# Kernel optimization log

Hardware: AMD Instinct MI355X
Metric: run time of the kernel (lower is better)

## Reference

```python
import jax, jax.numpy as jnp
import numpy as np

PART = 0  # index of '<PART>' tag in vocab (select_part_tag = zeros)
W = 3     # max_word_len


def lstm_scan(x_seq, h0, c0, Wih, Whh, bih, bhh):
    """x_seq: [S, N, D] -> outputs [S, N, H]. torch LSTM gate order i, f, g, o."""
    def cell(carry, x):
        h, c = carry
        g = x @ Wih.T + bih + h @ Whh.T + bhh
        i, f, gg, o = jnp.split(g, 4, axis=-1)
        c = jax.nn.sigmoid(f) * c + jax.nn.sigmoid(i) * jnp.tanh(gg)
        h = jax.nn.sigmoid(o) * jnp.tanh(c)
        return (h, c), h
    _, hs = jax.lax.scan(cell, (h0, c0), x_seq)
    return hs


def decoder_probs(win, h0, emb, Wih, Whh, bih, bhh, Wp, bp):
    """Decoder.forward for all start positions at once.
    win: [N, W] candidate-word tokens; h0: [N, H] (used as both h0 and c0).
    Returns [W, N]: row y = log p(word win[:, :y+1] then <PART>)."""
    N = win.shape[0]
    toks = jnp.concatenate([jnp.full((N, 1), PART, win.dtype), win], axis=1)  # prepend <PART>
    x = jnp.swapaxes(emb[toks], 0, 1)                    # [W+1, N, D]
    hs = lstm_scan(x, h0, h0, Wih, Whh, bih, bhh)        # [W+1, N, H]
    logits = hs @ Wp.T + bp                              # [W+1, N, V]
    logZ = jax.nn.logsumexp(logits, axis=-1)             # [W+1, N]
    # log_softmax gathered at target char / <PART> tag positions
    char = jnp.take_along_axis(logits[:-1], win.T[:, :, None], axis=-1)[..., 0] - logZ[:-1]  # [W, N]
    tag = logits[1:, :, PART] - logZ[1:]                 # [W, N]
    return jnp.cumsum(char, axis=0) + tag                # cumulative char logprob + end tag


def forward_loss(sentence, emb, enc, decf, decb):
    B, T = sentence.shape
    H = enc[1].shape[1]
    fvec = sentence
    bvec = jnp.flip(sentence, axis=1)

    def encode(vec):
        toks = jnp.concatenate([jnp.full((B, 1), PART, vec.dtype), vec[:, :-1]], axis=1)
        x = jnp.swapaxes(emb[toks], 0, 1)                # [T, B, D]
        z = jnp.zeros((B, H), emb.dtype)
        return lstm_scan(x, z, z, *enc)                  # [T, B, H]

    enc_f, enc_b = encode(fvec), encode(bvec)
    idx = jnp.clip(jnp.arange(T)[:, None] + jnp.arange(W)[None, :], 0, T - 1)  # [T, W]

    def run_dec(vec, enc_out, params):
        win = vec[:, idx].reshape(B * T, W)              # window starting at each position
        h0 = jnp.swapaxes(enc_out, 0, 1).reshape(B * T, -1)
        p = decoder_probs(win, h0, emb, *params)         # [W, B*T]
        return p.reshape(W, B, T).transpose(2, 0, 1)     # [T(start), W(len-1), B]

    fwdP = run_dec(fvec, enc_f, decf)
    bwdP = run_dec(bvec, enc_b, decb)

    xs = jnp.arange(T)[:, None]
    ys = jnp.arange(W)[None, :]
    # SGB_A.add_bidirection: P[x, y, b] = score of word of length y+1 ending at position x
    P = 0.5 * (fwdP[jnp.clip(xs - ys, 0, T - 1), ys] + bwdP[T - 1 - xs, ys])  # [T, W, B]

    # compute_all_probability: semi-CRF forward recursion
    NEG = jnp.asarray(-1e30, P.dtype)
    def step(buf, inp):
        # buf[i] = total[j-1-i]
        p_j, j = inp
        cand = jnp.where((jnp.arange(W) < j)[:, None], buf + p_j, NEG)
        tot = jax.nn.logsumexp(cand, axis=0)
        return jnp.concatenate([tot[None], buf[:-1]], axis=0), tot

    _, totals = jax.lax.scan(step, jnp.zeros((W, B), P.dtype), (P, jnp.arange(1, T + 1)))
    return -jnp.mean(totals[-1])


def setup_inputs() -> dict:
    key = jax.random.key(0)
    V, D, H, B, T = 8000, 256, 256, 16, 128
    ks = jax.random.split(key, 24)
    s_d = 1.0 / np.sqrt(D)
    s_h = 1.0 / np.sqrt(H)

    def mat(k, shape, scale):
        return jax.random.normal(k, shape, jnp.float32) * scale

    def lstm_p(k):
        k1, k2, k3, k4 = jax.random.split(k, 4)
        return (mat(k1, (4 * H, D), s_d), mat(k2, (4 * H, H), s_h),
                mat(k3, (4 * H,), s_h), mat(k4, (4 * H,), s_h))

    enc = lstm_p(ks[1])
    decf_l = lstm_p(ks[2])
    decb_l = lstm_p(ks[3])
    inp = {
        "sentence": jax.random.randint(ks[0], (B, T), 0, V, jnp.int32),
        "emb": mat(ks[4], (V, D), 1.0),
        "enc_Wih": enc[0], "enc_Whh": enc[1], "enc_bih": enc[2], "enc_bhh": enc[3],
        "decf_Wih": decf_l[0], "decf_Whh": decf_l[1], "decf_bih": decf_l[2], "decf_bhh": decf_l[3],
        "decf_Wp": mat(ks[5], (V, H), s_h), "decf_bp": mat(ks[6], (V,), s_h),
        "decb_Wih": decb_l[0], "decb_Whh": decb_l[1], "decb_bih": decb_l[2], "decb_bhh": decb_l[3],
        "decb_Wp": mat(ks[7], (V, H), s_h), "decb_bp": mat(ks[8], (V,), s_h),
    }
    return inp


def reference(sentence, emb, enc_Wih, enc_Whh, enc_bih, enc_bhh,
              decf_Wih, decf_Whh, decf_bih, decf_bhh, decf_Wp, decf_bp,
              decb_Wih, decb_Whh, decb_bih, decb_bhh, decb_Wp, decb_bp):
    return forward_loss(
        sentence, emb,
        (enc_Wih, enc_Whh, enc_bih, enc_bhh),
        (decf_Wih, decf_Whh, decf_bih, decf_bhh, decf_Wp, decf_bp),
        (decb_Wih, decb_Whh, decb_bih, decb_bhh, decb_Wp, decb_bp))
```

## Files before the change

kernel.cpp:

```cpp
#include <hip/hip_runtime.h>
#include <math.h>

#define VOCAB 8000
#define NN 2048

typedef unsigned short u16;
typedef __attribute__((ext_vector_type(8))) short short8v;
typedef __attribute__((ext_vector_type(4))) short short4v;
typedef __attribute__((ext_vector_type(4))) float float4v;
typedef __attribute__((ext_vector_type(4))) int int4v;

#define OFF_WPBF   0ul
#define OFF_WDEC   2048000ul
#define OFF_XENC   2572288ul
#define OFF_H0BF   4153344ul
#define OFF_DECX   4677632ul
#define OFF_CDEC   6250496ul
#define OFF_HSBF   7299072ul
#define OFF_GBUF   9396224ul
#define OFF_LOGZ   13590528ul
#define OFF_GCH    13606912ul
#define OFF_GTG    13619200ul
#define OFF_P      13631488ul
#define OFF_WTOK   13637632ul
#define OFF_XP0    13649920ul
#define OFF_ENCW   13652032ul
#define OFF_SENC   13914240ul
#define OFF_SQ     13915264ul
#define OFF_WQI8   13916288ul

__device__ __forceinline__ float sigf(float x) { return 1.0f / (1.0f + __expf(-x)); }
__device__ __forceinline__ float tanhsafe(float x) {
    x = fminf(15.0f, fmaxf(-15.0f, x));
    float e = __expf(2.0f * x);
    return (e - 1.0f) / (e + 1.0f);
}
__device__ __forceinline__ u16 f2bf(float f) {
    union { float f; unsigned int u; } x; x.f = f;
    return (u16)((x.u + 0x7fffu + ((x.u >> 16) & 1u)) >> 16);
}
__device__ __forceinline__ float bf2f(u16 x) {
    union { unsigned int u; float f; } v; v.u = ((unsigned int)x) << 16;
    return v.f;
}

__device__ __forceinline__ short8v ldfrag(const u16* lds, int row, int k, int lane, int SB) {
    int r = row + (lane & 15);
    int off = r * SB + ((k + ((lane >> 4) << 3)) << 1);
    off ^= (r & 7) << 4;
    return *(const short8v*)((const char*)lds + off);
}

__device__ __forceinline__ void stage128x256(const u16* __restrict__ g, int row0, int rowmax,
                                             int rowstride, int col0, u16* lds, int tid) {
    #pragma unroll
    for (int it = 0; it < 16; ++it) {
        int chunk = tid + it * 256;
        int r = chunk >> 5;
        int kc = (chunk & 31) << 3;
        short8v v = {0, 0, 0, 0, 0, 0, 0, 0};
        if (row0 + r < rowmax)
            v = *(const short8v*)(g + (size_t)(row0 + r) * rowstride + col0 + kc);
        int off = (r * 512 + kc * 2) ^ ((r & 7) << 4);
        *(short8v*)((char*)lds + off) = v;
    }
}


__global__ __launch_bounds__(256) void k_wpbf(const float* __restrict__ Wf,
                                              const float* __restrict__ Wb,
                                              u16* __restrict__ out) {
    int chunk = blockIdx.x * 256 + threadIdx.x;
    int kc = (chunk & 31) << 3;
    int v = (chunk >> 5) % 8000;
    int d = chunk / (8000 * 32);
    const float* src = (d ? Wb : Wf) + (size_t)v * 256 + kc;
    u16 t8[8];
    #pragma unroll
    for (int j = 0; j < 8; ++j) t8[j] = f2bf(src[j]);
    *(short8v*)(out + ((size_t)d * 8000 + v) * 256 + kc) = *(short8v*)t8;
}

__global__ __launch_bounds__(256) void k_wdecbf(const float* __restrict__ fWhh, const float* __restrict__ fWih,
                                                const float* __restrict__ bWhh, const float* __restrict__ bWih,
                                                u16* __restrict__ out) {
    int chunk = blockIdx.x * 256 + threadIdx.x;
    int kc = (chunk & 63) << 3;
    int r = (chunk >> 6) & 1023;
    int d = chunk >> 16;
    const float* Whh = d ? bWhh : fWhh;
    const float* Wih = d ? bWih : fWih;
    const float* src = (kc < 256) ? (Whh + (size_t)r * 256 + kc) : (Wih + (size_t)r * 256 + (kc - 256));
    u16 t8[8];
    #pragma unroll
    for (int j = 0; j < 8; ++j) t8[j] = f2bf(src[j]);
    *(short8v*)(out + ((size_t)d * 1024 + r) * 512 + kc) = *(short8v*)t8;
}

__global__ __launch_bounds__(256) void k_wencbf(const float* __restrict__ Whh, const float* __restrict__ Wih,
                                                u16* __restrict__ out) {
    int chunk = blockIdx.x * 256 + threadIdx.x;
    int kc = (chunk & 63) << 3;
    int r = chunk >> 6;
    const float* src = (kc < 256) ? (Whh + (size_t)r * 256 + kc) : (Wih + (size_t)r * 256 + (kc - 256));
    u16 t8[8];
    #pragma unroll
    for (int j = 0; j < 8; ++j) t8[j] = f2bf(src[j]);
    *(short8v*)(out + (size_t)r * 512 + kc) = *(short8v*)t8;
}

__global__ __launch_bounds__(256) void k_escale(const float* __restrict__ Whh,
                                                float* __restrict__ s_enc,
                                                float* __restrict__ sq) {
    int r = blockIdx.x * 256 + threadIdx.x;
    if (r >= 1024) return;
    float m = 0.0f;
    for (int k = 0; k < 256; ++k) m = fmaxf(m, fabsf(Whh[r * 256 + k]));
    s_enc[r] = m / 16129.0f;
    sq[r] = (m > 0.0f) ? 127.0f / m : 0.0f;
}

__global__ __launch_bounds__(256) void k_wq2(const float* __restrict__ Whh,
                                             const float* __restrict__ sq,
                                             signed char* __restrict__ wq) {
    int lin = blockIdx.x * 256 + threadIdx.x;
    int lane = lin & 63;
    int ks = (lin >> 6) & 3;
    int c = (lin >> 8) & 3;
    int w = lin >> 10;
    int r = c * 256 + w * 16 + (lane & 15);
    int kb = ks * 64 + ((lane >> 4) << 4);
    float s = sq[r];
    signed char o16[16];
    #pragma unroll
    for (int j = 0; j < 16; ++j) {
        float q = rintf(Whh[r * 256 + kb + j] * s);
        q = fminf(127.0f, fmaxf(-127.0f, q));
        o16[j] = (signed char)q;
    }
    *(int4v*)(wq + (size_t)lin * 16) = *(int4v*)o16;
}

__global__ __launch_bounds__(256) void k_xenc(const int* __restrict__ S, const float* __restrict__ emb,
                                              u16* __restrict__ out) {
    int chunk = blockIdx.x * 256 + threadIdx.x;
    int kc = (chunk & 31) << 3;
    int b = (chunk >> 5) & 15;
    int t = (chunk >> 9) & 127;
    int d = chunk >> 16;
    int tok = 0;
    if (t > 0) tok = d ? S[b * 128 + 128 - t] : S[b * 128 + t - 1];
    const float* src = emb + (size_t)tok * 256 + kc;
    u16 t8[8];
    #pragma unroll
    for (int j = 0; j < 8; ++j) t8[j] = f2bf(src[j]);
    *(short8v*)(out + (size_t)(((d * 128 + t) * 16) + b) * 256 + kc) = *(short8v*)t8;
}

__global__ __launch_bounds__(256) void k_decx(const int* __restrict__ S, const float* __restrict__ emb,
                                              u16* __restrict__ decX, int* __restrict__ winTok) {
    int chunk = blockIdx.x * 256 + threadIdx.x;
    int kc = (chunk & 31) << 3;
    int n = (chunk >> 5) & 2047;
    int r2 = chunk >> 16;
    int s = r2 % 3, d = r2 / 3;
    int b = n >> 7, tq = n & 127;
    int pos = min(tq + s, 127);
    int tok = d ? S[b * 128 + 127 - pos] : S[b * 128 + pos];
    const float* src = emb + (size_t)tok * 256 + kc;
    u16 t8[8];
    #pragma unroll
    for (int j = 0; j < 8; ++j) t8[j] = f2bf(src[j]);
    *(short8v*)(decX + ((size_t)(d * 3 + s) * NN + n) * 256 + kc) = *(short8v*)t8;
    if ((chunk & 31) == 0) winTok[(d * 3 + s) * NN + n] = tok;
}

__global__ __launch_bounds__(256) void k_xp0(const float* __restrict__ emb,
                                             const float* __restrict__ Wihf,
                                             const float* __restrict__ Wihb,
                                             float* __restrict__ xp0) {
    int idx = blockIdx.x * 256 + threadIdx.x;
    int d = idx >> 10, r = idx & 1023;
    const float* Wih = d ? Wihb : Wihf;
    float acc = 0.0f;
    for (int k = 0; k < 256; ++k) acc = fmaf(emb[k], Wih[r * 256 + k], acc);
    xp0[idx] = acc;
}

__global__ __launch_bounds__(256) void k_xproj(const u16* __restrict__ xEncBF,
                                               const u16* __restrict__ encW,
                                               const float* __restrict__ ebih,
                                               const float* __restrict__ ebhh,
                                               float* __restrict__ xpT) {
    __shared__ u16 At[128 * 256];
    __shared__ u16 Bt[128 * 256];
    const int tid = threadIdx.x, lane = tid & 63, wid = tid >> 6;
    const int wm = wid >> 1, wv = wid & 1;
    const int r0 = blockIdx.x * 128, n0 = blockIdx.y * 128, d = blockIdx.z;
    stage128x256(xEncBF + (size_t)d * 2048 * 256, n0, 1 << 30, 256, 0, At, tid);
    stage128x256(encW, r0, 1 << 30, 512, 256, Bt, tid);
    __syncthreads();
    float4v acc[4][4];
    #pragma unroll
    for (int m = 0; m < 4; ++m)
        #pragma unroll
        for (int v = 0; v < 4; ++v) acc[m][v] = (float4v){0.f, 0.f, 0.f, 0.f};
    #pragma unroll
    for (int k = 0; k < 8; ++k) {
        short8v af[4], bf[4];
        #pragma unroll
        for (int m = 0; m < 4; ++m) af[m] = ldfrag(At, wm * 64 + m * 16, k * 32, lane, 512);
        #pragma unroll
        for (int v = 0; v < 4; ++v) bf[v] = ldfrag(Bt, wv * 64 + v * 16, k * 32, lane, 512);
        #pragma unroll
        for (int m = 0; m < 4; ++m)
            #pragma unroll
            for (int v = 0; v < 4; ++v)
                acc[m][v] = __builtin_amdgcn_mfma_f32_16x16x32_bf16(af[m], bf[v], acc[m][v], 0, 0, 0);
    }
    float bs[4]; int rg[4];
    #pragma unroll
    for (int v = 0; v < 4; ++v) {
        rg[v] = r0 + wv * 64 + v * 16 + (lane & 15);
        bs[v] = ebih[rg[v]] + ebhh[rg[v]];
    }
    #pragma unroll
    for (int m = 0; m < 4; ++m)
        #pragma unroll
        for (int i = 0; i < 4; ++i) {
            int n = n0 + wm * 64 + m * 16 + ((lane >> 4) << 2) + i;
            int t_ = n >> 4, bfull = n & 15;
            #pragma unroll
            for (int v = 0; v < 4; ++v) {
                int g = rg[v] >> 8, u = rg[v] & 255;
                size_t idx4 = (((size_t)(d * 16 + bfull) * 128 + t_) * 16 + (u >> 4)) * 16 + (u & 15);
                xpT[idx4 * 4 + g] = acc[m][v][i] + bs[v];
            }
        }
}

__global__ __launch_bounds__(1024) void k_enc5(const signed char* __restrict__ wq,
                                               const float* __restrict__ s_enc,
                                               const float4v* __restrict__ xpT4,
                                               u16* __restrict__ h0bf) {
    __shared__ signed char hbuf[2][4096];
    const int tid = threadIdx.x, lane = tid & 63, w = tid >> 6;
    const int blk = blockIdx.x, d = blk >> 4, b = blk & 15;
    const int l15 = lane & 15, hi = lane >> 4;
    int4v breg[4][4];
    #pragma unroll
    for (int c = 0; c < 4; ++c)
        #pragma unroll
        for (int ks = 0; ks < 4; ++ks)
            breg[c][ks] = *(const int4v*)(wq + ((size_t)(((w * 4 + c) * 4 + ks) * 64 + lane)) * 16);
    float sreg[4];
    #pragma unroll
    for (int c = 0; c < 4; ++c) sreg[c] = s_enc[c * 256 + w * 16 + l15];
    float creg = 0.0f;
    ((long*)hbuf)[tid] = 0l;
    const bool cellane = (lane < 16);
    const int u = w * 16 + l15;
    const float4v* xbase = xpT4 + ((size_t)(d * 16 + b) * 128) * 256 + w * 16 + l15;
    float4v xv_next = {0.f, 0.f, 0.f, 0.f};
    if (cellane) xv_next = xbase[0];
    __syncthreads();
    for (int t = 0; t < 128; ++t) {
        int cur = t & 1;
        float4v xv = xv_next;
        if (cellane && t < 127) xv_next = xbase[(size_t)(t + 1) * 256];
        int4v af[4];
        #pragma unroll
        for (int ks = 0; ks < 4; ++ks) {
            int off = (l15 * 256 + ks * 64 + hi * 16) ^ ((l15 & 7) << 4);
            af[ks] = *(const int4v*)(hbuf[cur] + off);
        }
        int4v acc[4];
        #pragma unroll
        for (int c = 0; c < 4; ++c) {
            acc[c] = (int4v){0, 0, 0, 0};
            #pragma unroll
            for (int ks = 0; ks < 4; ++ks)
                acc[c] = __builtin_amdgcn_mfma_i32_16x16x64_i8(af[ks], breg[c][ks], acc[c], 0, 0, 0);
        }
        if (cellane) {
            float gi = (float)acc[0][0] * sreg[0] + xv[0];
            float gf = (float)acc[1][0] * sreg[1] + xv[1];
            float gG = (float)acc[2][0] * sreg[2] + xv[2];
            float go = (float)acc[3][0] * sreg[3] + xv[3];
            float cn = sigf(gf) * creg + sigf(gi) * tanhsafe(gG);
            float h = sigf(go) * tanhsafe(cn);
            creg = cn;
            h0bf[((size_t)d * NN + b * 128 + t) * 256 + u] = f2bf(h);
            hbuf[cur ^ 1][u] = (signed char)rintf(h * 127.0f);
        }
        __syncthreads();
    }
}

__global__ __launch_bounds__(256) void k_decmm(const u16* __restrict__ Ah, size_t ahStride,
                                               const u16* __restrict__ Axx, size_t axStride,
                                               const u16* __restrict__ Wdec,
                                               const float* __restrict__ bihf, const float* __restrict__ bhhf,
                                               const float* __restrict__ bihb, const float* __restrict__ bhhb,
                                               const float* __restrict__ xp0, int useX,
                                               float* __restrict__ gBuf) {
    __shared__ u16 At[128 * 256];
    __shared__ u16 Bt[128 * 256];
    const int tid = threadIdx.x, lane = tid & 63, wid = tid >> 6;
    const int wm = wid >> 1, wv = wid & 1;
    const int r0 = blockIdx.x * 128, n0 = blockIdx.y * 128, d = blockIdx.z;
    float4v acc[4][4];
    #pragma unroll
    for (int m = 0; m < 4; ++m)
        #pragma unroll
        for (int v = 0; v < 4; ++v) acc[m][v] = (float4v){0.f, 0.f, 0.f, 0.f};
    const int nph = useX ? 2 : 1;
    for (int ph = 0; ph < nph; ++ph) {
        const u16* Asrc = (ph == 0) ? (Ah + (size_t)d * ahStride) : (Axx + (size_t)d * axStride);
        stage128x256(Asrc, n0, 1 << 30, 256, 0, At, tid);
        stage128x256(Wdec + (size_t)d * 1024 * 512, r0, 1 << 30, 512, ph * 256, Bt, tid);
        __syncthreads();
        #pragma unroll
        for (int k = 0; k < 8; ++k) {
            short8v af[4], bf[4];
            #pragma unroll
            for (int m = 0; m < 4; ++m) af[m] = ldfrag(At, wm * 64 + m * 16, k * 32, lane, 512);
            #pragma unroll
            for (int v = 0; v < 4; ++v) bf[v] = ldfrag(Bt, wv * 64 + v * 16, k * 32, lane, 512);
            #pragma unroll
            for (int m = 0; m < 4; ++m)
                #pragma unroll
                for (int v = 0; v < 4; ++v)
                    acc[m][v] = __builtin_amdgcn_mfma_f32_16x16x32_bf16(af[m], bf[v], acc[m][v], 0, 0, 0);
        }
        __syncthreads();
    }
    const float* bih = d ? bihb : bihf;
    const float* bhh = d ? bhhb : bhhf;
    float bs[4]; int rg[4];
    #pragma unroll
    for (int v = 0; v < 4; ++v) {
        rg[v] = r0 + wv * 64 + v * 16 + (lane & 15);
        bs[v] = bih[rg[v]] + bhh[rg[v]];
        if (!useX) bs[v] += xp0[d * 1024 + rg[v]];
    }
    #pragma unroll
    for (int m = 0; m < 4; ++m)
        #pragma unroll
        for (int i = 0; i < 4; ++i) {
            int n = n0 + wm * 64 + m * 16 + ((lane >> 4) << 2) + i;
            #pragma unroll
            for (int v = 0; v < 4; ++v)
                gBuf[((size_t)d * NN + n) * 1024 + rg[v]] = acc[m][v][i] + bs[v];
        }
}

__global__ __launch_bounds__(256) void k_deccell(const float* __restrict__ gBuf,
                                                 const u16* __restrict__ h0bf,
                                                 float* __restrict__ cDec,
                                                 u16* __restrict__ hsBF, int s) {
    int flat = blockIdx.x * 256 + threadIdx.x;
    int j = flat & 255;
    int n = (flat >> 8) & 2047;
    int d = flat >> 19;
    const float* g = gBuf + ((size_t)d * NN + n) * 1024;
    float gi = g[j], gf = g[j + 256], gg = g[j + 512], go = g[j + 768];
    float cprev = (s == 0) ? bf2f(h0bf[flat]) : cDec[flat];
    float cn = sigf(gf) * cprev + sigf(gi) * tanhsafe(gg);
    float h = sigf(go) * tanhsafe(cn);
    cDec[flat] = cn;
    hsBF[((size_t)(d * 4 + s) * NN + n) * 256 + j] = f2bf(h);
}

__global__ __launch_bounds__(512, 4) void k_proj3(const u16* __restrict__ hsBF,
                                                  const u16* __restrict__ WpBF,
                                                  const float* __restrict__ bpf, const float* __restrict__ bpb,
                                                  const int* __restrict__ winTok,
                                                  float* __restrict__ partials,
                                                  float* __restrict__ gchar, float* __restrict__ gtag) {
    __shared__ u16 Bt[64 * 256];
    __shared__ u16 Ab[128 * 128];
    const int tid = threadIdx.x, lane = tid & 63, w = tid >> 6;
    const int l15 = lane & 15, hi = lane >> 4;
    const int n0 = blockIdx.x * 128, vt = blockIdx.y, d = blockIdx.z;
    const int v0 = vt * 64;
    const float* bp = d ? bpb : bpf;
    float bpv[4]; int vg[4];
    #pragma unroll
    for (int v = 0; v < 4; ++v) {
        vg[v] = v0 + v * 16 + l15;
        bpv[v] = bp[vg[v]];
    }

#define LOADA3(s_, h_) do {                                                       \
        const u16* hsA = hsBF + (size_t)(d * 4 + (s_)) * NN * 256;                \
        _Pragma("unroll")                                                         \
        for (int it = 0; it < 4; ++it) {                                          \
            int g = tid + it * 512; int r = g >> 4, kc = (g & 15) << 3;           \
            areg[it] = *(const short8v*)(hsA + (size_t)(n0 + r) * 256 + (h_) * 128 + kc); \
        }                                                                         \
    } while (0)
#define WRITEA3() do {                                                            \
        _Pragma("unroll")                                                         \
        for (int it = 0; it < 4; ++it) {                                          \
            int g = tid + it * 512; int r = g >> 4, kc = (g & 15) << 3;           \
            int off = (r * 256 + kc * 2) ^ ((r & 7) << 4);                        \
            *(short8v*)((char*)Ab + off) = areg[it];                              \
        }                                                                         \
    } while (0)

    #pragma unroll
    for (int it = 0; it < 4; ++it) {
        int g = tid + it * 512; int r = g >> 5, kc = (g & 31) << 3;
        short8v bv = *(const short8v*)(WpBF + ((size_t)d * 8000 + v0 + r) * 256 + kc);
        int off = (r * 512 + kc * 2) ^ ((r & 7) << 4);
        *(short8v*)((char*)Bt + off) = bv;
    }
    short8v areg[4];
    LOADA3(0, 0);

    for (int s = 0; s < 4; ++s) {
        float4v acc[4];
        #pragma unroll
        for (int v = 0; v < 4; ++v) acc[v] = (float4v){0.f, 0.f, 0.f, 0.f};
        #pragma unroll
        for (int h = 0; h < 2; ++h) {
            WRITEA3();
            __syncthreads();
            if (!(s == 3 && h == 1)) {
                int ns = (h == 1) ? s + 1 : s, nh = h ^ 1;
                LOADA3(ns, nh);
            }
            #pragma unroll
            for (int kk = 0; kk < 4; ++kk) {
                short8v af = ldfrag(Ab, w * 16, kk * 32, lane, 256);
                short8v bf[4];
                #pragma unroll
                for (int v = 0; v < 4; ++v)
                    bf[v] = ldfrag(Bt, v * 16, h * 128 + kk * 32, lane, 512);
                #pragma unroll
                for (int v = 0; v < 4; ++v)
                    acc[v] = __builtin_amdgcn_mfma_f32_16x16x32_bf16(af, bf[v], acc[v], 0, 0, 0);
            }
            if (h == 0) __syncthreads();
        }
        #pragma unroll
        for (int i = 0; i < 4; ++i) {
            int n = n0 + w * 16 + hi * 4 + i;
            int tok = (s < 3) ? winTok[(d * 3 + s) * NN + n] : -1;
            float lg[4];
            #pragma unroll
            for (int v = 0; v < 4; ++v) {
                lg[v] = acc[v][i] + bpv[v];
                if (vg[v] == tok) gchar[(d * 3 + s) * NN + n] = lg[v];
                if (s >= 1 && vg[v] == 0) gtag[(d * 3 + (s - 1)) * NN + n] = lg[v];
            }
            float mx = fmaxf(fmaxf(lg[0], lg[1]), fmaxf(lg[2], lg[3]));
            #pragma unroll
            for (int off = 1; off <= 8; off <<= 1) mx = fmaxf(mx, __shfl_xor(mx, off));
            float sum = 0.0f;
            #pragma unroll
            for (int v = 0; v < 4; ++v) sum += __expf(lg[v] - mx);
            #pragma unroll
            for (int off = 1; off <= 8; off <<= 1) sum += __shfl_xor(sum, off);
            if (l15 == 0)
                partials[((size_t)(d * 4 + s) * NN + n) * 128 + vt] = mx + __logf(sum);
        }
        __syncthreads();
    }
#undef LOADA3
#undef WRITEA3
}

__global__ __launch_bounds__(256) void k_lzred(const float* __restrict__ partials,
                                               float* __restrict__ logZ) {
    int wid = threadIdx.x >> 6, lane = threadIdx.x & 63;
    int row = blockIdx.x * 4 + wid;
    const float* p = partials + (size_t)row * 128;
    float mx = p[lane];
    float sum = 1.0f;
    if (lane + 64 < 125) {
        float b = p[lane + 64];
        float M = fmaxf(mx, b);
        sum = __expf(mx - M) + __expf(b - M);
        mx = M;
    }
    #pragma unroll
    for (int off = 1; off <= 32; off <<= 1) {
        float m2 = __shfl_xor(mx, off);
        float s2 = __shfl_xor(sum, off);
        float M = fmaxf(mx, m2);
        sum = sum * __expf(mx - M) + s2 * __expf(m2 - M);
        mx = M;
    }
    if (lane == 0) logZ[row] = mx + __logf(sum);
}

__global__ __launch_bounds__(256) void k_passm(const float* __restrict__ gchar,
                                               const float* __restrict__ gtag,
                                               const float* __restrict__ logZ,
                                               float* __restrict__ P) {
    int flat = blockIdx.x * 256 + threadIdx.x;
    if (flat >= 128 * 3 * 16) return;
    int b = flat & 15;
    int y = (flat >> 4) % 3;
    int x = flat / 48;
    int nf = b * 128 + min(127, max(0, x - y));
    int nb = b * 128 + 127 - x;
    float pf = 0.0f, pb = 0.0f;
    for (int ss = 0; ss <= y; ++ss) {
        pf += gchar[ss * NN + nf] - logZ[ss * NN + nf];
        pb += gchar[(3 + ss) * NN + nb] - logZ[(4 + ss) * NN + nb];
    }
    pf += gtag[y * NN + nf] - logZ[(y + 1) * NN + nf];
    pb += gtag[(3 + y) * NN + nb] - logZ[(4 + y + 1) * NN + nb];
    P[flat] = 0.5f * (pf + pb);
}

__global__ __launch_bounds__(64) void k_scan(const float* __restrict__ P, float* __restrict__ out) {
    __shared__ float buf[3][16];
    __shared__ float cand[3][16];
    __shared__ float tot[16];
    int tid = threadIdx.x;
    if (tid < 48) buf[tid / 16][tid % 16] = 0.0f;
    __syncthreads();
    for (int j = 1; j <= 128; ++j) {
        if (tid < 48) {
            int i = tid / 16, b = tid % 16;
            cand[i][b] = (i < j) ? buf[i][b] + P[((j - 1) * 3 + i) * 16 + b] : -1e30f;
        }
        __syncthreads();
        if (tid < 16) {
            int b = tid;
            float c0 = cand[0][b], c1 = cand[1][b], c2 = cand[2][b];
            float mx = fmaxf(c0, fmaxf(c1, c2));
            float sv = __expf(c0 - mx) + __expf(c1 - mx) + __expf(c2 - mx);
            float t_ = mx + __logf(sv);
            float b0 = buf[0][b], b1 = buf[1][b];
            buf[0][b] = t_; buf[1][b] = b0; buf[2][b] = b1;
            tot[b] = t_;
        }
        __syncthreads();
    }
    if (tid == 0) {
        float sacc = 0.0f;
        for (int b = 0; b < 16; ++b) sacc += tot[b];
        out[0] = -sacc / 16.0f;
    }
}

extern "C" void kernel_launch(void* const* d_in, const int* in_sizes, int n_in,
                              void* d_out, int out_size, void* d_ws, size_t ws_size,
                              hipStream_t stream) {
    const int* S = (const int*)d_in[0];
    const float* emb = (const float*)d_in[1];
    const float* eWih = (const float*)d_in[2];
    const float* eWhh = (const float*)d_in[3];
    const float* ebih = (const float*)d_in[4];
    const float* ebhh = (const float*)d_in[5];
    const float* fWih = (const float*)d_in[6];
    const float* fWhh = (const float*)d_in[7];
    const float* fbih = (const float*)d_in[8];
    const float* fbhh = (const float*)d_in[9];
    const float* fWp  = (const float*)d_in[10];
    const float* fbp  = (const float*)d_in[11];
    const float* bWih = (const float*)d_in[12];
    const float* bWhh = (const float*)d_in[13];
    const float* bbih = (const float*)d_in[14];
    const float* bbhh = (const float*)d_in[15];
    const float* bWp  = (const float*)d_in[16];
    const float* bbp  = (const float*)d_in[17];

    float* w = (float*)d_ws;
    u16* WpBF    = (u16*)(w + OFF_WPBF);
    u16* WdecBF  = (u16*)(w + OFF_WDEC);
    u16* xEncBF  = (u16*)(w + OFF_XENC);
    u16* h0bf    = (u16*)(w + OFF_H0BF);
    u16* decXBF  = (u16*)(w + OFF_DECX);
    float* cDec  = w + OFF_CDEC;
    u16* hsBF    = (u16*)(w + OFF_HSBF);
    float* gBuf  = w + OFF_GBUF;
    float* xpT   = gBuf;
    float* partials = gBuf;
    float* logZ  = w + OFF_LOGZ;
    float* gchar = w + OFF_GCH;
    float* gtag  = w + OFF_GTG;
    float* Pm    = w + OFF_P;
    int* winTok  = (int*)(w + OFF_WTOK);
    float* xp0   = w + OFF_XP0;
    u16* encW    = (u16*)(w + OFF_ENCW);
    float* sEnc  = w + OFF_SENC;
    float* sQ    = w + OFF_SQ;
    signed char* wqEnc = (signed char*)(w + OFF_WQI8);

    k_wpbf<<<2000, 256, 0, stream>>>(fWp, bWp, WpBF);
    k_wdecbf<<<512, 256, 0, stream>>>(fWhh, fWih, bWhh, bWih, WdecBF);
    k_wencbf<<<256, 256, 0, stream>>>(eWhh, eWih, encW);
    k_escale<<<4, 256, 0, stream>>>(eWhh, sEnc, sQ);
    k_wq2<<<64, 256, 0, stream>>>(eWhh, sQ, wqEnc);
    k_xenc<<<512, 256, 0, stream>>>(S, emb, xEncBF);
    k_decx<<<1536, 256, 0, stream>>>(S, emb, decXBF, winTok);
    k_xp0<<<8, 256, 0, stream>>>(emb, fWih, bWih, xp0);

    k_xproj<<<dim3(8, 16, 2), 256, 0, stream>>>(xEncBF, encW, ebih, ebhh, xpT);
    k_enc5<<<32, 1024, 0, stream>>>(wqEnc, sEnc, (const float4v*)xpT, h0bf);

    for (int s = 0; s < 4; ++s) {
        const u16* Ah; size_t ahS;
        const u16* Axx; size_t axS;
        if (s == 0) {
            Ah = h0bf; ahS = (size_t)NN * 256;
            Axx = decXBF; axS = (size_t)3 * NN * 256;
        } else {
            Ah = hsBF + (size_t)(s - 1) * NN * 256; ahS = (size_t)4 * NN * 256;
            Axx = decXBF + (size_t)(s - 1) * NN * 256; axS = (size_t)3 * NN * 256;
        }
        k_decmm<<<dim3(8, 16, 2), 256, 0, stream>>>(Ah, ahS, Axx, axS, WdecBF,
                                                    fbih, fbhh, bbih, bbhh, xp0,
                                                    (s == 0) ? 0 : 1, gBuf);
        k_deccell<<<4096, 256, 0, stream>>>(gBuf, h0bf, cDec, hsBF, s);
    }

    k_proj3<<<dim3(16, 125, 2), 512, 0, stream>>>(hsBF, WpBF, fbp, bbp, winTok,
                                                  partials, gchar, gtag);
    k_lzred<<<4096, 256, 0, stream>>>(partials, logZ);
    k_passm<<<24, 256, 0, stream>>>(gchar, gtag, logZ, Pm);
    k_scan<<<1, 64, 0, stream>>>(Pm, (float*)d_out);
}
```

Before: 581.6 us.

## Restructure vocab projection to loop over vocab chunks with unshifted exp-sum partials

The projection kernel now keeps a full 128x256 hidden tile in LDS and loops over 16 vocab tiles per block, double-buffering the Wp tiles. This replaces the grid of 125 vocab tiles that each reloaded the A tile. The softmax partials become plain sums of exp(logit) without max-shifting, so the logZ reduction reduces to 16 additions and a log. This drops many per-tile max shuffles and cuts the partials traffic, but risks overflow if logits are large. The final scan also moves to a single-warp register recurrence with the P matrix preloaded into LDS, removing the per-step barriers.

```diff
diff --git a/kernel.cpp b/kernel.cpp
--- a/kernel.cpp
+++ b/kernel.cpp
@@ -372,128 +372,132 @@
     hsBF[((size_t)(d * 4 + s) * NN + n) * 256 + j] = f2bf(h);
 }
 
-__global__ __launch_bounds__(512, 4) void k_proj3(const u16* __restrict__ hsBF,
-                                                  const u16* __restrict__ WpBF,
-                                                  const float* __restrict__ bpf, const float* __restrict__ bpb,
-                                                  const int* __restrict__ winTok,
-                                                  float* __restrict__ partials,
-                                                  float* __restrict__ gchar, float* __restrict__ gtag) {
-    __shared__ u16 Bt[64 * 256];
-    __shared__ u16 Ab[128 * 128];
+__global__ __launch_bounds__(512) void k_proj4(const u16* __restrict__ hsBF,
+                                               const u16* __restrict__ WpBF,
+                                               const float* __restrict__ bpf, const float* __restrict__ bpb,
+                                               const int* __restrict__ winTok,
+                                               float* __restrict__ partials,
+                                               float* __restrict__ gchar, float* __restrict__ gtag) {
+    __shared__ u16 At[128 * 256];
+    __shared__ u16 Bt[2][64 * 256];
     const int tid = threadIdx.x, lane = tid & 63, w = tid >> 6;
+    const int wm = w >> 1, wv = w & 1;
     const int l15 = lane & 15, hi = lane >> 4;
-    const int n0 = blockIdx.x * 128, vt = blockIdx.y, d = blockIdx.z;
-    const int v0 = vt * 64;
+    const int n0 = blockIdx.x * 128, chunkI = blockIdx.y, d = blockIdx.z;
+    const int vt0 = chunkI * 16;
+    const int nvt = min(16, 125 - vt0);
     const float* bp = d ? bpb : bpf;
-    float bpv[4]; int vg[4];
-    #pragma unroll
-    for (int v = 0; v < 4; ++v) {
-        vg[v] = v0 + v * 16 + l15;
-        bpv[v] = bp[vg[v]];
-    }
-
-#define LOADA3(s_, h_) do {                                                       \
-        const u16* hsA = hsBF + (size_t)(d * 4 + (s_)) * NN * 256;                \
+
+#define LOADB4(vt_) do {                                                          \
         _Pragma("unroll")                                                         \
         for (int it = 0; it < 4; ++it) {                                          \
-            int g = tid + it * 512; int r = g >> 4, kc = (g & 15) << 3;           \
-            areg[it] = *(const short8v*)(hsA + (size_t)(n0 + r) * 256 + (h_) * 128 + kc); \
+            int g = tid + it * 512; int r = g >> 5, kc = (g & 31) << 3;           \
+            bregs[it] = *(const short8v*)(WpBF + ((size_t)d * 8000 + (vt_) * 64 + r) * 256 + kc); \
         }                                                                         \
     } while (0)
-#define WRITEA3() do {                                                            \
+#define WRITEB4(buf_) do {                                                        \
         _Pragma("unroll")                                                         \
         for (int it = 0; it < 4; ++it) {                                          \
-            int g = tid + it * 512; int r = g >> 4, kc = (g & 15) << 3;           \
-            int off = (r * 256 + kc * 2) ^ ((r & 7) << 4);                        \
-            *(short8v*)((char*)Ab + off) = areg[it];                              \
+            int g = tid + it * 512; int r = g >> 5, kc = (g & 31) << 3;           \
+            int off = (r * 512 + kc * 2) ^ ((r & 7) << 4);                        \
+            *(short8v*)((char*)Bt[buf_] + off) = bregs[it];                       \
         }                                                                         \
     } while (0)
 
-    #pragma unroll
-    for (int it = 0; it < 4; ++it) {
-        int g = tid + it * 512; int r = g >> 5, kc = (g & 31) << 3;
-        short8v bv = *(const short8v*)(WpBF + ((size_t)d * 8000 + v0 + r) * 256 + kc);
-        int off = (r * 512 + kc * 2) ^ ((r & 7) << 4);
-        *(short8v*)((char*)Bt + off) = bv;
-    }
-    short8v areg[4];
-    LOADA3(0, 0);
-
+    short8v bregs[4];
     for (int s = 0; s < 4; ++s) {
-        float4v acc[4];
-        #pragma unroll
-        for (int v = 0; v < 4; ++v) acc[v] = (float4v){0.f, 0.f, 0.f, 0.f};
-        #pragma unroll
-        for (int h = 0; h < 2; ++h) {
-            WRITEA3();
+        const u16* hsA = hsBF + (size_t)(d * 4 + s) * NN * 256;
+        #pragma unroll
+        for (int it = 0; it < 8; ++it) {
+            int chunk = tid + it * 512;
+            int r = chunk >> 5, kc = (chunk & 31) << 3;
+            short8v v8 = *(const short8v*)(hsA + (size_t)(n0 + r) * 256 + kc);
+            int off = (r * 512 + kc * 2) ^ ((r & 7) << 4);
+            *(short8v*)((char*)At + off) = v8;
+        }
+        LOADB4(vt0);
+        WRITEB4(0);
+        int tok[2][4];
+        #pragma unroll
+        for (int m = 0; m < 2; ++m)
+            #pragma unroll
+            for (int i = 0; i < 4; ++i) {
+                int n = n0 + wm * 32 + m * 16 + hi * 4 + i;
+                tok[m][i] = (s < 3) ? winTok[(d * 3 + s) * NN + n] : -1;
+            }
+        float expsum[2][4] = {{0.f, 0.f, 0.f, 0.f}, {0.f, 0.f, 0.f, 0.f}};
+        __syncthreads();
+        int cur = 0;
+        for (int t = 0; t < nvt; ++t) {
+            int vt = vt0 + t;
+            if (t + 1 < nvt) LOADB4(vt + 1);
+            float bpv[2];
+            #pragma unroll
+            for (int v = 0; v < 2; ++v) bpv[v] = bp[vt * 64 + wv * 32 + v * 16 + l15];
+            float4v acc[2][2];
+            #pragma unroll
+            for (int m = 0; m < 2; ++m)
+                #pragma unroll
+                for (int v = 0; v < 2; ++v) acc[m][v] = (float4v){0.f, 0.f, 0.f, 0.f};
+            #pragma unroll
+            for (int kk = 0; kk < 8; ++kk) {
+                short8v af[2], bf[2];
+                #pragma unroll
+                for (int m = 0; m < 2; ++m) af[m] = ldfrag(At, wm * 32 + m * 16, kk * 32, lane, 512);
+                #pragma unroll
+                for (int v = 0; v < 2; ++v) bf[v] = ldfrag(Bt[cur], wv * 32 + v * 16, kk * 32, lane, 512);
+                #pragma unroll
+                for (int m = 0; m < 2; ++m)
+                    #pragma unroll
+                    for (int v = 0; v < 2; ++v)
+                        acc[m][v] = __builtin_amdgcn_mfma_f32_16x16x32_bf16(af[m], bf[v], acc[m][v], 0, 0, 0);
+            }
+            #pragma unroll
+            for (int m = 0; m < 2; ++m)
+                #pragma unroll
+                for (int i = 0; i < 4; ++i) {
+                    int n = n0 + wm * 32 + m * 16 + hi * 4 + i;
+                    float es = 0.0f;
+                    #pragma unroll
+                    for (int v = 0; v < 2; ++v) {
+                        int vgv = vt * 64 + wv * 32 + v * 16 + l15;
+                        float lg = acc[m][v][i] + bpv[v];
+                        es += __expf(lg);
+                        if (vgv == tok[m][i]) gchar[(d * 3 + s) * NN + n] = lg;
+                        if (s >= 1 && vgv == 0) gtag[(d * 3 + (s - 1)) * NN + n] = lg;
+                    }
+                    expsum[m][i] += es;
+                }
             __syncthreads();
-            if (!(s == 3 && h == 1)) {
-                int ns = (h == 1) ? s + 1 : s, nh = h ^ 1;
-                LOADA3(ns, nh);
+            if (t + 1 < nvt) WRITEB4(cur ^ 1);
+            __syncthreads();
+            cur ^= 1;
+        }
+        #pragma unroll
+        for (int m = 0; m < 2; ++m)
+            #pragma unroll
+            for (int i = 0; i < 4; ++i) {
+                float e = expsum[m][i];
+                #pragma unroll
+                for (int off = 1; off <= 8; off <<= 1) e += __shfl_xor(e, off);
+                if (l15 == 0) {
+                    int n = n0 + wm * 32 + m * 16 + hi * 4 + i;
+                    partials[((size_t)(d * 4 + s) * NN + n) * 16 + chunkI * 2 + wv] = e;
+                }
             }
-            #pragma unroll
-            for (int kk = 0; kk < 4; ++kk) {
-                short8v af = ldfrag(Ab, w * 16, kk * 32, lane, 256);
-                short8v bf[4];
-                #pragma unroll
-                for (int v = 0; v < 4; ++v)
-                    bf[v] = ldfrag(Bt, v * 16, h * 128 + kk * 32, lane, 512);
-                #pragma unroll
-                for (int v = 0; v < 4; ++v)
-                    acc[v] = __builtin_amdgcn_mfma_f32_16x16x32_bf16(af, bf[v], acc[v], 0, 0, 0);
-            }
-            if (h == 0) __syncthreads();
-        }
-        #pragma unroll
-        for (int i = 0; i < 4; ++i) {
-            int n = n0 + w * 16 + hi * 4 + i;
-            int tok = (s < 3) ? winTok[(d * 3 + s) * NN + n] : -1;
-            float lg[4];
-            #pragma unroll
-            for (int v = 0; v < 4; ++v) {
-                lg[v] = acc[v][i] + bpv[v];
-                if (vg[v] == tok) gchar[(d * 3 + s) * NN + n] = lg[v];
-                if (s >= 1 && vg[v] == 0) gtag[(d * 3 + (s - 1)) * NN + n] = lg[v];
-            }
-            float mx = fmaxf(fmaxf(lg[0], lg[1]), fmaxf(lg[2], lg[3]));
-            #pragma unroll
-            for (int off = 1; off <= 8; off <<= 1) mx = fmaxf(mx, __shfl_xor(mx, off));
-            float sum = 0.0f;
-            #pragma unroll
-            for (int v = 0; v < 4; ++v) sum += __expf(lg[v] - mx);
-            #pragma unroll
-            for (int off = 1; off <= 8; off <<= 1) sum += __shfl_xor(sum, off);
-            if (l15 == 0)
-                partials[((size_t)(d * 4 + s) * NN + n) * 128 + vt] = mx + __logf(sum);
-        }
-        __syncthreads();
-    }
-#undef LOADA3
-#undef WRITEA3
-}
-
-__global__ __launch_bounds__(256) void k_lzred(const float* __restrict__ partials,
+    }
+#undef LOADB4
+#undef WRITEB4
+}
+
+__global__ __launch_bounds__(256) void k_lzsum(const float* __restrict__ partials,
                                                float* __restrict__ logZ) {
-    int wid = threadIdx.x >> 6, lane = threadIdx.x & 63;
-    int row = blockIdx.x * 4 + wid;
-    const float* p = partials + (size_t)row * 128;
-    float mx = p[lane];
-    float sum = 1.0f;
-    if (lane + 64 < 125) {
-        float b = p[lane + 64];
-        float M = fmaxf(mx, b);
-        sum = __expf(mx - M) + __expf(b - M);
-        mx = M;
-    }
-    #pragma unroll
-    for (int off = 1; off <= 32; off <<= 1) {
-        float m2 = __shfl_xor(mx, off);
-        float s2 = __shfl_xor(sum, off);
-        float M = fmaxf(mx, m2);
-        sum = sum * __expf(mx - M) + s2 * __expf(m2 - M);
-        mx = M;
-    }
-    if (lane == 0) logZ[row] = mx + __logf(sum);
+    int row = blockIdx.x * 256 + threadIdx.x;
+    const float* p = partials + (size_t)row * 16;
+    float s = 0.0f;
+    #pragma unroll
+    for (int c = 0; c < 16; ++c) s += p[c];
+    logZ[row] = __logf(s);
 }
 
 __global__ __launch_bounds__(256) void k_passm(const float* __restrict__ gchar,
@@ -518,34 +522,26 @@
 }
 
 __global__ __launch_bounds__(64) void k_scan(const float* __restrict__ P, float* __restrict__ out) {
-    __shared__ float buf[3][16];
-    __shared__ float cand[3][16];
-    __shared__ float tot[16];
+    __shared__ float Pl[128 * 48];
     int tid = threadIdx.x;
-    if (tid < 48) buf[tid / 16][tid % 16] = 0.0f;
+    #pragma unroll
+    for (int it = 0; it < 96; ++it) Pl[tid + it * 64] = P[tid + it * 64];
     __syncthreads();
-    for (int j = 1; j <= 128; ++j) {
-        if (tid < 48) {
-            int i = tid / 16, b = tid % 16;
-            cand[i][b] = (i < j) ? buf[i][b] + P[((j - 1) * 3 + i) * 16 + b] : -1e30f;
-        }
-        __syncthreads();
-        if (tid < 16) {
-            int b = tid;
-            float c0 = cand[0][b], c1 = cand[1][b], c2 = cand[2][b];
+    if (tid < 16) {
+        int b = tid;
+        float b0 = 0.f, b1 = 0.f, b2 = 0.f, tot = 0.f;
+        for (int j = 1; j <= 128; ++j) {
+            float c0 = b0 + Pl[((j - 1) * 3 + 0) * 16 + b];
+            float c1 = (j >= 2) ? b1 + Pl[((j - 1) * 3 + 1) * 16 + b] : -1e30f;
+            float c2 = (j >= 3) ? b2 + Pl[((j - 1) * 3 + 2) * 16 + b] : -1e30f;
             float mx = fmaxf(c0, fmaxf(c1, c2));
             float sv = __expf(c0 - mx) + __expf(c1 - mx) + __expf(c2 - mx);
-            float t_ = mx + __logf(sv);
-            float b0 = buf[0][b], b1 = buf[1][b];
-            buf[0][b] = t_; buf[1][b] = b0; buf[2][b] = b1;
-            tot[b] = t_;
-        }
-        __syncthreads();
-    }
-    if (tid == 0) {
-        float sacc = 0.0f;
-        for (int b = 0; b < 16; ++b) sacc += tot[b];
-        out[0] = -sacc / 16.0f;
+            tot = mx + __logf(sv);
+            b2 = b1; b1 = b0; b0 = tot;
+        }
+        #pragma unroll
+        for (int off = 1; off <= 8; off <<= 1) tot += __shfl_xor(tot, off);
+        if (b == 0) out[0] = -tot / 16.0f;
     }
 }
 
@@ -621,9 +617,9 @@
         k_deccell<<<4096, 256, 0, stream>>>(gBuf, h0bf, cDec, hsBF, s);
     }
 
-    k_proj3<<<dim3(16, 125, 2), 512, 0, stream>>>(hsBF, WpBF, fbp, bbp, winTok,
-                                                  partials, gchar, gtag);
-    k_lzred<<<4096, 256, 0, stream>>>(partials, logZ);
+    k_proj4<<<dim3(16, 8, 2), 512, 0, stream>>>(hsBF, WpBF, fbp, bbp, winTok,
+                                                partials, gchar, gtag);
+    k_lzsum<<<64, 256, 0, stream>>>(partials, logZ);
     k_passm<<<24, 256, 0, stream>>>(gchar, gtag, logZ, Pm);
     k_scan<<<1, 64, 0, stream>>>(Pm, (float*)d_out);
 }
```

Result: faster. 515.3 us (-11.4%).
